# Kernel tuning notes

Measured on AMD Instinct MI355X. Metric: run time of the kernel, lower is better.

## Reference

```python
import jax, jax.numpy as jnp
import numpy as np

B, S, D, DFF = 4, 2048, 1024, 4096
EPS = 1e-5


def layernorm(x, g, b):
    mu = jnp.mean(x, axis=-1, keepdims=True)
    var = jnp.mean(jnp.square(x - mu), axis=-1, keepdims=True)
    return (x - mu) * jax.lax.rsqrt(var + EPS) * g + b


def setup_inputs() -> dict:
    key = jax.random.key(0)
    ks = jax.random.split(key, 4)
    hidden_state = jax.random.normal(ks[0], (B, S, D), dtype=jnp.float32)
    attention_mask = jnp.zeros((B, 1, S), dtype=jnp.float32)  # additive mask
    w1 = jax.random.normal(ks[1], (D, DFF), dtype=jnp.float32) * (1.0 / np.sqrt(D))
    b1 = jnp.zeros((DFF,), dtype=jnp.float32)
    w2 = jax.random.normal(ks[2], (DFF, D), dtype=jnp.float32) * (1.0 / np.sqrt(DFF))
    b2 = jnp.zeros((D,), dtype=jnp.float32)
    ln1_g = jnp.ones((D,), dtype=jnp.float32)
    ln1_b = jnp.zeros((D,), dtype=jnp.float32)
    ln2_g = jnp.ones((D,), dtype=jnp.float32)
    ln2_b = jnp.zeros((D,), dtype=jnp.float32)
    return dict(hidden_state=hidden_state, attention_mask=attention_mask,
                w1=w1, b1=b1, w2=w2, b2=b2,
                ln1_g=ln1_g, ln1_b=ln1_b, ln2_g=ln2_g, ln2_b=ln2_b)


def reference(hidden_state, attention_mask, w1, b1, w2, b2, ln1_g, ln1_b, ln2_g, ln2_b):
    x = hidden_state
    d = jnp.asarray(x.shape[-1], x.dtype)
    # hand-rolled single-head attention: q=k=v=x (source forward ignores QKV projections)
    scores = jnp.einsum('bqd,bkd->bqk', x, x) / jnp.sqrt(d) + attention_mask  # [B,S,S]
    attn = jax.nn.softmax(scores, axis=-1)
    attn_out = jnp.einsum('bqk,bkd->bqd', attn, x)
    h = layernorm(x + attn_out, ln1_g, ln1_b)
    # FFN: dense -> exact GELU -> linear_2
    ffn = jnp.einsum('bsf,fd->bsd', jax.nn.gelu(jnp.einsum('bsd,df->bsf', h, w1) + b1, approximate=False), w2) + b2
    return layernorm(h + ffn, ln2_g, ln2_b)
```

## Files before the change

### kernel.cpp

```cpp
#include <hip/hip_runtime.h>
#include <hip/hip_bf16.h>
#include <math.h>

#define LN_EPS 1e-5f

typedef short short8 __attribute__((ext_vector_type(8)));
typedef float floatx4 __attribute__((ext_vector_type(4)));

__device__ inline unsigned short f2bf(float f) {
    unsigned int u = __float_as_uint(f);
    u += 0x7fff + ((u >> 16) & 1);
    return (unsigned short)(u >> 16);
}

__device__ inline void gl_lds16(const unsigned short* g, unsigned short* l) {
    __builtin_amdgcn_global_load_lds(
        (__attribute__((address_space(1))) const void*)g,
        (__attribute__((address_space(3))) void*)l, 16, 0, 0);
}

__device__ inline float gelu_f(float v) {
    float u2 = 2.0f * v * (0.7978845608f + 0.0356774081f * v * v);
    float t  = 1.0f - 2.0f / (__expf(u2) + 1.0f);
    return 0.5f * v * (1.0f + t);
}

template<int EPI>
__global__ __launch_bounds__(256) void gemm_bt(
    const unsigned short* __restrict__ A, const unsigned short* __restrict__ B,
    const float* __restrict__ bias, const float* __restrict__ resid,
    void* __restrict__ Cptr,
    int M, int N, int K, long sA, long sB, long sC, long sBias, float scale)
{
    __shared__ unsigned short lds_a[2 * 128 * 32];
    __shared__ unsigned short lds_b[2 * 128 * 32];

    const int tid  = threadIdx.x;
    const int lane = tid & 63;
    const int wave = tid >> 6;
    const int quad = lane >> 4;
    const int l16  = lane & 15;
    const int wm = wave >> 1, wn = wave & 1;
    const int tile_m = blockIdx.y * 128;
    const int tile_n = blockIdx.x * 128;
    const int batch  = blockIdx.z;

    const unsigned short* Ab = A + (size_t)batch * sA;
    const unsigned short* Bb = B + (size_t)batch * sB;

    const int srow = wave * 16 + (lane >> 2);
    const int scol = (lane & 3) * 8;
    const unsigned short* gA0 = Ab + (size_t)(tile_m + srow) * K + scol;
    const unsigned short* gA1 = Ab + (size_t)(tile_m + 64 + srow) * K + scol;
    const unsigned short* gB0 = Bb + (size_t)(tile_n + srow) * K + scol;
    const unsigned short* gB1 = Bb + (size_t)(tile_n + 64 + srow) * K + scol;
    unsigned short* lA0 = &lds_a[wave * 512 + lane * 8];
    unsigned short* lA1 = &lds_a[2048 + wave * 512 + lane * 8];
    unsigned short* lB0 = &lds_b[wave * 512 + lane * 8];
    unsigned short* lB1 = &lds_b[2048 + wave * 512 + lane * 8];

    floatx4 acc[4][4];
    const floatx4 zero = {0.f, 0.f, 0.f, 0.f};
#pragma unroll
    for (int i = 0; i < 4; i++)
#pragma unroll
        for (int j = 0; j < 4; j++) acc[i][j] = zero;

    for (int k0 = 0; k0 < K; k0 += 64) {
        __syncthreads();
        gl_lds16(gA0 + k0, lA0);
        gl_lds16(gA1 + k0, lA1);
        gl_lds16(gB0 + k0, lB0);
        gl_lds16(gB1 + k0, lB1);
        gl_lds16(gA0 + k0 + 32, lA0 + 4096);
        gl_lds16(gA1 + k0 + 32, lA1 + 4096);
        gl_lds16(gB0 + k0 + 32, lB0 + 4096);
        gl_lds16(gB1 + k0 + 32, lB1 + 4096);
        __syncthreads();

#pragma unroll
        for (int h = 0; h < 2; h++) {
            short8 afr[4], bfr[4];
#pragma unroll
            for (int i = 0; i < 4; i++)
                afr[i] = *(const short8*)
                    &lds_a[h * 4096 + (wm * 64 + i * 16 + l16) * 32 + quad * 8];
#pragma unroll
            for (int j = 0; j < 4; j++)
                bfr[j] = *(const short8*)
                    &lds_b[h * 4096 + (wn * 64 + j * 16 + l16) * 32 + quad * 8];
#pragma unroll
            for (int i = 0; i < 4; i++)
#pragma unroll
                for (int j = 0; j < 4; j++)
                    acc[i][j] = __builtin_amdgcn_mfma_f32_16x16x32_bf16(
                        bfr[j], afr[i], acc[i][j], 0, 0, 0);
        }
    }

#pragma unroll
    for (int i = 0; i < 4; i++) {
        const int row = tile_m + wm * 64 + i * 16 + l16;
#pragma unroll
        for (int j = 0; j < 4; j++) {
            const int colb = tile_n + wn * 64 + j * 16 + quad * 4;
            float v[4];
#pragma unroll
            for (int r = 0; r < 4; r++) v[r] = acc[i][j][r];

            if (EPI == 3) {
                float4 mv = *(const float4*)&bias[(size_t)batch * sBias + colb];
                v[0] = v[0] * scale + mv.x;  v[1] = v[1] * scale + mv.y;
                v[2] = v[2] * scale + mv.z;  v[3] = v[3] * scale + mv.w;
            }
            if (EPI == 2 || EPI == 5) {
                float4 bv = *(const float4*)&bias[colb];
                v[0] += bv.x; v[1] += bv.y; v[2] += bv.z; v[3] += bv.w;
            }
            if (EPI == 2) {
#pragma unroll
                for (int r = 0; r < 4; r++) v[r] = gelu_f(v[r]);
            }
            if (EPI == 4 || EPI == 5) {
                float4 rv = *(const float4*)&resid[(size_t)batch * sC +
                                                   (size_t)row * N + colb];
                v[0] += rv.x; v[1] += rv.y; v[2] += rv.z; v[3] += rv.w;
            }

            if (EPI == 2 || EPI == 3) {
                unsigned short* C = (unsigned short*)Cptr + (size_t)batch * sC;
                ushort4 h4;
                h4.x = f2bf(v[0]); h4.y = f2bf(v[1]);
                h4.z = f2bf(v[2]); h4.w = f2bf(v[3]);
                *(ushort4*)(C + (size_t)row * N + colb) = h4;
            } else {
                float* C = (float*)Cptr + (size_t)batch * sC;
                float4 f4 = {v[0], v[1], v[2], v[3]};
                *(float4*)(C + (size_t)row * N + colb) = f4;
            }
        }
    }
}

__global__ __launch_bounds__(256) void x_prep_kernel(
    const float* __restrict__ in, unsigned short* __restrict__ straight,
    unsigned short* __restrict__ transposed, int R, int C, long sIn)
{
    __shared__ float tile[32][33];
    const int tc = blockIdx.x * 32, tr = blockIdx.y * 32;
    const float* src = in + (size_t)blockIdx.z * sIn;
    unsigned short* dstS = straight   + (size_t)blockIdx.z * sIn;
    unsigned short* dstT = transposed + (size_t)blockIdx.z * sIn;
    const int tx = threadIdx.x & 31, ty = threadIdx.x >> 5;
#pragma unroll
    for (int i = 0; i < 4; i++) {
        float val = src[(size_t)(tr + ty + i * 8) * C + tc + tx];
        tile[ty + i * 8][tx] = val;
        dstS[(size_t)(tr + ty + i * 8) * C + tc + tx] = f2bf(val);
    }
    __syncthreads();
#pragma unroll
    for (int i = 0; i < 4; i++)
        dstT[(size_t)(tc + ty + i * 8) * R + tr + tx] = f2bf(tile[tx][ty + i * 8]);
}

__global__ __launch_bounds__(256) void transpose_cvt_kernel(
    const float* __restrict__ in, unsigned short* __restrict__ out, int R, int C)
{
    __shared__ float tile[32][33];
    const int tc = blockIdx.x * 32, tr = blockIdx.y * 32;
    const int tx = threadIdx.x & 31, ty = threadIdx.x >> 5;
#pragma unroll
    for (int i = 0; i < 4; i++)
        tile[ty + i * 8][tx] = in[(size_t)(tr + ty + i * 8) * C + tc + tx];
    __syncthreads();
#pragma unroll
    for (int i = 0; i < 4; i++)
        out[(size_t)(tc + ty + i * 8) * R + tr + tx] = f2bf(tile[tx][ty + i * 8]);
}

__global__ __launch_bounds__(256) void softmax_bf16_kernel(
    const unsigned short* __restrict__ scores, unsigned short* __restrict__ probs,
    int S)
{
    __shared__ float red[4];
    const int row = blockIdx.x;
    const unsigned short* p = scores + (size_t)row * S;
    unsigned short* pr      = probs  + (size_t)row * S;
    const int tid  = threadIdx.x;
    const int lane = tid & 63;
    const int wav  = tid >> 6;

    uint4 raw = *(const uint4*)(p + tid * 8);
    float v[8];
    v[0] = __uint_as_float(raw.x << 16); v[1] = __uint_as_float(raw.x & 0xffff0000u);
    v[2] = __uint_as_float(raw.y << 16); v[3] = __uint_as_float(raw.y & 0xffff0000u);
    v[4] = __uint_as_float(raw.z << 16); v[5] = __uint_as_float(raw.z & 0xffff0000u);
    v[6] = __uint_as_float(raw.w << 16); v[7] = __uint_as_float(raw.w & 0xffff0000u);

    float mx = v[0];
#pragma unroll
    for (int k = 1; k < 8; k++) mx = fmaxf(mx, v[k]);
#pragma unroll
    for (int off = 32; off > 0; off >>= 1) mx = fmaxf(mx, __shfl_down(mx, off));
    if (lane == 0) red[wav] = mx;
    __syncthreads();
    mx = fmaxf(fmaxf(red[0], red[1]), fmaxf(red[2], red[3]));
    __syncthreads();

    float s = 0.f;
#pragma unroll
    for (int k = 0; k < 8; k++) { v[k] = __expf(v[k] - mx); s += v[k]; }
#pragma unroll
    for (int off = 32; off > 0; off >>= 1) s += __shfl_down(s, off);
    if (lane == 0) red[wav] = s;
    __syncthreads();
    s = red[0] + red[1] + red[2] + red[3];
    float inv = 1.0f / s;

    uint4 o;
    o.x = (unsigned)f2bf(v[0] * inv) | ((unsigned)f2bf(v[1] * inv) << 16);
    o.y = (unsigned)f2bf(v[2] * inv) | ((unsigned)f2bf(v[3] * inv) << 16);
    o.z = (unsigned)f2bf(v[4] * inv) | ((unsigned)f2bf(v[5] * inv) << 16);
    o.w = (unsigned)f2bf(v[6] * inv) | ((unsigned)f2bf(v[7] * inv) << 16);
    *(uint4*)(pr + tid * 8) = o;
}

template<int WRITE_BF16>
__global__ __launch_bounds__(256) void ln_kernel(
    const float* __restrict__ X,
    const float* __restrict__ g, const float* __restrict__ bta,
    float* __restrict__ out, unsigned short* __restrict__ out16, int D)
{
    __shared__ float red[8];
    const int row = blockIdx.x;
    const float* x = X + (size_t)row * D;
    const int tid  = threadIdx.x;
    const int lane = tid & 63;
    const int wav  = tid >> 6;

    float4 a = *(const float4*)(x + tid * 4);
    float v0 = a.x, v1 = a.y, v2 = a.z, v3 = a.w;

    float s1 = v0 + v1 + v2 + v3;
    float s2 = v0 * v0 + v1 * v1 + v2 * v2 + v3 * v3;
#pragma unroll
    for (int off = 32; off > 0; off >>= 1) {
        s1 += __shfl_down(s1, off);
        s2 += __shfl_down(s2, off);
    }
    if (lane == 0) { red[wav] = s1; red[4 + wav] = s2; }
    __syncthreads();
    s1 = red[0] + red[1] + red[2] + red[3];
    s2 = red[4] + red[5] + red[6] + red[7];
    const float mu  = s1 / (float)D;
    const float var = s2 / (float)D - mu * mu;
    const float rs  = rsqrtf(var + LN_EPS);

    float4 gg = *(const float4*)(g + tid * 4);
    float4 bb = *(const float4*)(bta + tid * 4);
    float4 r;
    r.x = (v0 - mu) * rs * gg.x + bb.x;
    r.y = (v1 - mu) * rs * gg.y + bb.y;
    r.z = (v2 - mu) * rs * gg.z + bb.z;
    r.w = (v3 - mu) * rs * gg.w + bb.w;
    *(float4*)(out + (size_t)row * D + tid * 4) = r;
    if (WRITE_BF16) {
        ushort4 h;
        h.x = f2bf(r.x); h.y = f2bf(r.y); h.z = f2bf(r.z); h.w = f2bf(r.w);
        *(ushort4*)(out16 + (size_t)row * D + tid * 4) = h;
    }
}

extern "C" void kernel_launch(void* const* d_in, const int* in_sizes, int n_in,
                              void* d_out, int out_size, void* d_ws, size_t ws_size,
                              hipStream_t stream) {
    (void)in_sizes; (void)n_in; (void)out_size; (void)ws_size;
    const float* x    = (const float*)d_in[0];
    const float* mask = (const float*)d_in[1];
    const float* w1   = (const float*)d_in[2];
    const float* b1   = (const float*)d_in[3];
    const float* w2   = (const float*)d_in[4];
    const float* b2   = (const float*)d_in[5];
    const float* ln1g = (const float*)d_in[6];
    const float* ln1b = (const float*)d_in[7];
    const float* ln2g = (const float*)d_in[8];
    const float* ln2b = (const float*)d_in[9];
    float* out = (float*)d_out;

    const int B = 4, S = 2048, D = 1024, DFF = 4096;
    const size_t MB = 1024 * 1024;

    char* ws = (char*)d_ws;
    unsigned short* scoresb = (unsigned short*)ws;
    unsigned short* act     = (unsigned short*)ws;
    unsigned short* xb      = (unsigned short*)(ws + 32 * MB);
    unsigned short* probs   = (unsigned short*)(ws + 32 * MB);
    float*          hbuf    = (float*)(ws + 64 * MB);
    unsigned short* hb16    = (unsigned short*)(ws + 96 * MB);
    unsigned short* w1T     = (unsigned short*)(ws + 112 * MB);
    unsigned short* w2T     = (unsigned short*)(ws + 120 * MB);
    unsigned short* xTb     = (unsigned short*)d_out;
    float*          fsum    = (float*)d_out;

    x_prep_kernel<<<dim3(D / 32, S / 32, B), 256, 0, stream>>>(
        x, xb, xTb, S, D, (long)S * D);
    transpose_cvt_kernel<<<dim3(DFF / 32, D / 32, 1), 256, 0, stream>>>(w1, w1T, D, DFF);
    transpose_cvt_kernel<<<dim3(D / 32, DFF / 32, 1), 256, 0, stream>>>(w2, w2T, DFF, D);

    hipLaunchKernelGGL((gemm_bt<3>), dim3(S / 128, S / 128, B), dim3(256), 0, stream,
                       xb, xb, mask, (const float*)nullptr, (void*)scoresb,
                       S, S, D, (long)S * D, (long)S * D, (long)S * S, (long)S, 0.03125f);
    softmax_bf16_kernel<<<B * S, 256, 0, stream>>>(scoresb, probs, S);
    hipLaunchKernelGGL((gemm_bt<4>), dim3(D / 128, S / 128, B), dim3(256), 0, stream,
                       probs, xTb, (const float*)nullptr, x, (void*)hbuf,
                       S, D, S, (long)S * S, (long)D * S, (long)S * D, 0L, 0.f);
    hipLaunchKernelGGL((ln_kernel<1>), dim3(B * S), dim3(256), 0, stream,
                       hbuf, ln1g, ln1b, hbuf, hb16, D);
    hipLaunchKernelGGL((gemm_bt<2>), dim3(DFF / 128, (B * S) / 128, 1), dim3(256), 0, stream,
                       hb16, w1T, b1, (const float*)nullptr, (void*)act,
                       B * S, DFF, D, 0L, 0L, 0L, 0L, 0.f);
    hipLaunchKernelGGL((gemm_bt<5>), dim3(D / 128, (B * S) / 128, 1), dim3(256), 0, stream,
                       act, w2T, b2, hbuf, (void*)fsum,
                       B * S, D, DFF, 0L, 0L, 0L, 0L, 0.f);
    hipLaunchKernelGGL((ln_kernel<0>), dim3(B * S), dim3(256), 0, stream,
                       fsum, ln2g, ln2b, out, (unsigned short*)nullptr, D);
}
```

Measured before the change: 477.2 us.

## Load B operand fragments directly from global into registers with prefetch

The B tile no longer goes through LDS. Each wave loads its own B fragments straight from global memory into registers, double-buffered one K-step ahead, while A still goes through LDS. This cuts LDS traffic and halves LDS use, but B loads are now duplicated across the two waves sharing wn and are less coalesced. It also adds register pressure. The K loop is unrolled by two and assumes K is a multiple of 128.

```diff
diff --git a/kernel.cpp b/kernel.cpp
--- a/kernel.cpp
+++ b/kernel.cpp
@@ -33,7 +33,6 @@
     int M, int N, int K, long sA, long sB, long sC, long sBias, float scale)
 {
     __shared__ unsigned short lds_a[2 * 128 * 32];
-    __shared__ unsigned short lds_b[2 * 128 * 32];
 
     const int tid  = threadIdx.x;
     const int lane = tid & 63;
@@ -52,12 +51,13 @@
     const int scol = (lane & 3) * 8;
     const unsigned short* gA0 = Ab + (size_t)(tile_m + srow) * K + scol;
     const unsigned short* gA1 = Ab + (size_t)(tile_m + 64 + srow) * K + scol;
-    const unsigned short* gB0 = Bb + (size_t)(tile_n + srow) * K + scol;
-    const unsigned short* gB1 = Bb + (size_t)(tile_n + 64 + srow) * K + scol;
     unsigned short* lA0 = &lds_a[wave * 512 + lane * 8];
     unsigned short* lA1 = &lds_a[2048 + wave * 512 + lane * 8];
-    unsigned short* lB0 = &lds_b[wave * 512 + lane * 8];
-    unsigned short* lB1 = &lds_b[2048 + wave * 512 + lane * 8];
+
+    const unsigned short* gB[4];
+#pragma unroll
+    for (int j = 0; j < 4; j++)
+        gB[j] = Bb + (size_t)(tile_n + wn * 64 + j * 16 + l16) * K + quad * 8;
 
     floatx4 acc[4][4];
     const floatx4 zero = {0.f, 0.f, 0.f, 0.f};
@@ -66,36 +66,46 @@
 #pragma unroll
         for (int j = 0; j < 4; j++) acc[i][j] = zero;
 
-    for (int k0 = 0; k0 < K; k0 += 64) {
+    short8 b0[2][4], b1[2][4];
+#pragma unroll
+    for (int h = 0; h < 2; h++)
+#pragma unroll
+        for (int j = 0; j < 4; j++)
+            b0[h][j] = *(const short8*)(gB[j] + h * 32);
+
+    auto body = [&](short8 bcur[2][4], short8 bnext[2][4], int k0) {
         __syncthreads();
-        gl_lds16(gA0 + k0, lA0);
-        gl_lds16(gA1 + k0, lA1);
-        gl_lds16(gB0 + k0, lB0);
-        gl_lds16(gB1 + k0, lB1);
+        gl_lds16(gA0 + k0,      lA0);
+        gl_lds16(gA1 + k0,      lA1);
         gl_lds16(gA0 + k0 + 32, lA0 + 4096);
         gl_lds16(gA1 + k0 + 32, lA1 + 4096);
-        gl_lds16(gB0 + k0 + 32, lB0 + 4096);
-        gl_lds16(gB1 + k0 + 32, lB1 + 4096);
         __syncthreads();
-
+        if (k0 + 64 < K) {
+#pragma unroll
+            for (int h = 0; h < 2; h++)
+#pragma unroll
+                for (int j = 0; j < 4; j++)
+                    bnext[h][j] = *(const short8*)(gB[j] + k0 + 64 + h * 32);
+        }
 #pragma unroll
         for (int h = 0; h < 2; h++) {
-            short8 afr[4], bfr[4];
+            short8 afr[4];
 #pragma unroll
             for (int i = 0; i < 4; i++)
                 afr[i] = *(const short8*)
                     &lds_a[h * 4096 + (wm * 64 + i * 16 + l16) * 32 + quad * 8];
 #pragma unroll
-            for (int j = 0; j < 4; j++)
-                bfr[j] = *(const short8*)
-                    &lds_b[h * 4096 + (wn * 64 + j * 16 + l16) * 32 + quad * 8];
-#pragma unroll
             for (int i = 0; i < 4; i++)
 #pragma unroll
                 for (int j = 0; j < 4; j++)
                     acc[i][j] = __builtin_amdgcn_mfma_f32_16x16x32_bf16(
-                        bfr[j], afr[i], acc[i][j], 0, 0, 0);
+                        bcur[h][j], afr[i], acc[i][j], 0, 0, 0);
         }
+    };
+
+    for (int k0 = 0; k0 < K; k0 += 128) {
+        body(b0, b1, k0);
+        body(b1, b0, k0 + 64);
     }
 
 #pragma unroll
```

Result: slower. 665.1 us (+39.4%).
